# Performance work log

Hardware: AMD Instinct MI355X
Metric: run time of the kernel (lower is better)

The kernel has to match this reference:

```python
import jax, jax.numpy as jnp
import numpy as np

N_NODES = 100000
N_EDGES = 1600000
D_IN = 64
H = 64


def setup_inputs() -> dict:
    key = jax.random.key(0)
    ks = jax.random.split(key, 8)
    inp = {
        "x": jax.random.normal(ks[0], (N_NODES, D_IN), dtype=jnp.float32),
        "edge_index": jax.random.randint(ks[1], (2, N_EDGES), 0, N_NODES, dtype=jnp.int64),
        # layer 1 (SAGEConv): lin_l (aggregated neighbors, with bias), lin_r (root, no bias)
        "Wl1": jax.random.normal(ks[2], (D_IN, H), dtype=jnp.float32) / np.sqrt(D_IN),
        "bl1": jnp.zeros((H,), dtype=jnp.float32),
        "Wr1": jax.random.normal(ks[3], (D_IN, H), dtype=jnp.float32) / np.sqrt(D_IN),
        # layer 2
        "Wl2": jax.random.normal(ks[4], (H, H), dtype=jnp.float32) / np.sqrt(H),
        "bl2": jnp.zeros((H,), dtype=jnp.float32),
        "Wr2": jax.random.normal(ks[5], (H, H), dtype=jnp.float32) / np.sqrt(H),
        "Wfc": jax.random.normal(ks[6], (H, 1), dtype=jnp.float32) / np.sqrt(H),
        "bfc": jnp.zeros((1,), dtype=jnp.float32),
    }
    return inp


def _sage_conv(h, src, dst, inv_deg, Wl, bl, Wr):
    # mean-aggregate neighbor features: scatter-add messages then normalize by in-degree
    agg = jax.ops.segment_sum(h[src], dst, num_segments=N_NODES)  # [N, d]
    agg = agg * inv_deg[:, None]
    return agg @ Wl + bl + h @ Wr


def reference(x, edge_index, Wl1, bl1, Wr1, Wl2, bl2, Wr2, Wfc, bfc):
    src, dst = edge_index[0], edge_index[1]
    deg = jax.ops.segment_sum(jnp.ones((src.shape[0],), dtype=x.dtype), dst,
                              num_segments=N_NODES)
    inv_deg = jnp.where(deg > 0, 1.0 / jnp.maximum(deg, 1.0), 0.0)

    h = jax.nn.relu(_sage_conv(x, src, dst, inv_deg, Wl1, bl1, Wr1))
    h = jax.nn.relu(_sage_conv(h, src, dst, inv_deg, Wl2, bl2, Wr2))
    return h @ Wfc + bfc  # [N, 1]
```

## Files before the change

kernel.cpp:

```cpp
#include <hip/hip_runtime.h>
#include <hip/hip_fp16.h>

#define NN 100000
#define NE 1600000
#define SHIFT 8
#define NBUCK 391
#define P1B   391
#define EPB   4093

typedef _Float16 f16x8 __attribute__((ext_vector_type(8)));
typedef float f32x4 __attribute__((ext_vector_type(4)));
union H8U4 { f16x8 h; uint4 u; };

__device__ __forceinline__ int scan256(int* s, int t, int v) {
    s[t] = v;
    __syncthreads();
    for (int off = 1; off < 256; off <<= 1) {
        int add = (t >= off) ? s[t - off] : 0;
        __syncthreads();
        s[t] += add;
        __syncthreads();
    }
    return s[t];
}

__global__ __launch_bounds__(256) void k_hist(
    const float4* __restrict__ x4, ushort4* __restrict__ xh4,
    const float* __restrict__ Wl1, const float* __restrict__ Wr1, unsigned short* __restrict__ wt1,
    const float* __restrict__ Wl2, const float* __restrict__ Wr2, unsigned short* __restrict__ wt2,
    const int* __restrict__ dst, int* __restrict__ hist, int* __restrict__ bin_total)
{
    __shared__ int h[NBUCK];
    int t = threadIdx.x, blk = blockIdx.x;

    const int n4 = NN * 16;
    const int per = (n4 + P1B - 1) / P1B;
    int cb = blk * per, ce = min(cb + per, n4);
    for (int i = cb + t; i < ce; i += 256) {
        float4 f = x4[i];
        _Float16 a = (_Float16)f.x, b = (_Float16)f.y, c = (_Float16)f.z, d = (_Float16)f.w;
        ushort4 u;
        u.x = *(unsigned short*)&a; u.y = *(unsigned short*)&b;
        u.z = *(unsigned short*)&c; u.w = *(unsigned short*)&d;
        xh4[i] = u;
    }
    if (blk < 64) {
        int idx = (blk & 31) * 256 + t;
        const float* Wl = (blk < 32) ? Wl1 : Wl2;
        const float* Wr = (blk < 32) ? Wr1 : Wr2;
        unsigned short* wt = (blk < 32) ? wt1 : wt2;
        int n = idx >> 7, k = idx & 127;
        float v = (k < 64) ? Wl[k * 64 + n] : Wr[(k - 64) * 64 + n];
        _Float16 hv = (_Float16)v;
        wt[idx] = *(unsigned short*)&hv;
    }

    for (int i = t; i < NBUCK; i += 256) h[i] = 0;
    __syncthreads();
    int eb = blk * EPB, ee = min(eb + EPB, NE);
    for (int e = eb + t; e < ee; e += 256) atomicAdd(&h[dst[e] >> SHIFT], 1);
    __syncthreads();
    for (int i = t; i < NBUCK; i += 256) {
        int v = h[i];
        hist[(size_t)i * P1B + blk] = v;
        if (v) atomicAdd(&bin_total[i], v);
    }
}

__global__ __launch_bounds__(256) void k_cursor(int* __restrict__ hist, const int* __restrict__ bin_total,
                                                int* __restrict__ bucket_start, int* __restrict__ offsets) {
    __shared__ int sS[256];
    int b = blockIdx.x, t = threadIdx.x;

    int v = 0;
    for (int i = t; i < b; i += 256) v += bin_total[i];
    sS[t] = v;
    __syncthreads();
    for (int s = 128; s > 0; s >>= 1) {
        if (t < s) sS[t] += sS[t + s];
        __syncthreads();
    }
    int base = sS[0];
    __syncthreads();
    if (t == 0) bucket_start[b] = base;
    if (b == 0 && t == 0) { bucket_start[NBUCK] = NE; offsets[NN] = NE; }

    int carry = 0;
#pragma unroll
    for (int c = 0; c < 2; c++) {
        int idx = c * 256 + t;
        int hv = (idx < P1B) ? hist[(size_t)b * P1B + idx] : 0;
        int incl = scan256(sS, t, hv);
        if (idx < P1B) hist[(size_t)b * P1B + idx] = base + carry + incl - hv;
        __syncthreads();
        carry += sS[255];
        __syncthreads();
    }
}

__global__ __launch_bounds__(256) void k_scatter(const int* __restrict__ src, const int* __restrict__ dst,
                                                 const int* __restrict__ hist, unsigned int* __restrict__ pairs) {
    __shared__ int cur[NBUCK];
    int t = threadIdx.x, blk = blockIdx.x;
    for (int i = t; i < NBUCK; i += 256) cur[i] = hist[(size_t)i * P1B + blk];
    __syncthreads();
    int eb = blk * EPB, ee = min(eb + EPB, NE);
    for (int e = eb + t; e < ee; e += 256) {
        int d = dst[e];
        int pos = atomicAdd(&cur[d >> SHIFT], 1);
        pairs[pos] = (unsigned int)src[e] | ((unsigned int)(d & 255) << 17);
    }
}

__global__ __launch_bounds__(256) void k_bucket_csr(const unsigned int* __restrict__ pairs,
                                                    const int* __restrict__ bucket_start,
                                                    int* __restrict__ ssrc, int* __restrict__ offsets,
                                                    float* __restrict__ inv_deg) {
    __shared__ int cnt[256];
    __shared__ int sS[256];
    int b = blockIdx.x, t = threadIdx.x;
    cnt[t] = 0;
    __syncthreads();
    int beg = bucket_start[b], end = bucket_start[b + 1];
    for (int e = beg + t; e < end; e += 256) atomicAdd(&cnt[pairs[e] >> 17], 1);
    __syncthreads();
    int deg = cnt[t];
    int incl = scan256(sS, t, deg);
    int ex = incl - deg;
    int node = (b << SHIFT) + t;
    if (node < NN) {
        offsets[node] = beg + ex;
        inv_deg[node] = (deg > 0) ? (1.0f / (float)deg) : 0.0f;
    }
    __syncthreads();
    cnt[t] = beg + ex;
    __syncthreads();
    for (int e = beg + t; e < end; e += 256) {
        unsigned int pr = pairs[e];
        int pos = atomicAdd(&cnt[pr >> 17], 1);
        ssrc[pos] = (int)(pr & 0x1FFFFu);
    }
}

__global__ __launch_bounds__(256) void k_aggregate(const uint4* __restrict__ featq,
                                                   const int* __restrict__ ssrc,
                                                   const int* __restrict__ offsets, const float* __restrict__ inv_deg,
                                                   uint4* __restrict__ outq) {
    int pairid = blockIdx.x * 4 + (threadIdx.x >> 6);
    int node0 = pairid * 2;
    if (node0 >= NN) return;
    int node1 = node0 + 1;
    bool has1 = node1 < NN;
    int lane = threadIdx.x & 63;
    int c = lane & 7, g = lane >> 3;

    int beg0 = offsets[node0], end0 = offsets[node0 + 1];
    int beg1 = has1 ? offsets[node1] : 0, end1 = has1 ? offsets[node1 + 1] : 0;
    H8U4 acc0, acc1;
    acc0.h = (f16x8)(_Float16)0;
    acc1.h = (f16x8)(_Float16)0;
    int e0 = beg0, e1 = beg1;

    while (e0 + 16 <= end0 && e1 + 16 <= end1) {
        int i00 = ssrc[e0 + g], i01 = ssrc[e0 + 8 + g];
        int i10 = ssrc[e1 + g], i11 = ssrc[e1 + 8 + g];
        H8U4 q00, q01, q10, q11;
        q00.u = featq[(size_t)i00 * 8 + c];
        q01.u = featq[(size_t)i01 * 8 + c];
        q10.u = featq[(size_t)i10 * 8 + c];
        q11.u = featq[(size_t)i11 * 8 + c];
        acc0.h += q00.h; acc0.h += q01.h;
        acc1.h += q10.h; acc1.h += q11.h;
        e0 += 16; e1 += 16;
    }
    for (; e0 + 16 <= end0; e0 += 16) {
        int i0 = ssrc[e0 + g], i1 = ssrc[e0 + 8 + g];
        H8U4 q0, q1;
        q0.u = featq[(size_t)i0 * 8 + c];
        q1.u = featq[(size_t)i1 * 8 + c];
        acc0.h += q0.h; acc0.h += q1.h;
    }
    for (; e0 < end0; e0 += 8) {
        int m = end0 - e0;
        int idx = ssrc[e0 + (g < m ? g : m - 1)];
        H8U4 q;
        q.u = featq[(size_t)idx * 8 + c];
        if (g < m) acc0.h += q.h;
    }
    for (; e1 + 16 <= end1; e1 += 16) {
        int i0 = ssrc[e1 + g], i1 = ssrc[e1 + 8 + g];
        H8U4 q0, q1;
        q0.u = featq[(size_t)i0 * 8 + c];
        q1.u = featq[(size_t)i1 * 8 + c];
        acc1.h += q0.h; acc1.h += q1.h;
    }
    for (; e1 < end1; e1 += 8) {
        int m = end1 - e1;
        int idx = ssrc[e1 + (g < m ? g : m - 1)];
        H8U4 q;
        q.u = featq[(size_t)idx * 8 + c];
        if (g < m) acc1.h += q.h;
    }

#pragma unroll
    for (int mask = 8; mask <= 32; mask <<= 1) {
        H8U4 o0, o1;
        o0.u.x = __shfl_xor(acc0.u.x, mask); o0.u.y = __shfl_xor(acc0.u.y, mask);
        o0.u.z = __shfl_xor(acc0.u.z, mask); o0.u.w = __shfl_xor(acc0.u.w, mask);
        o1.u.x = __shfl_xor(acc1.u.x, mask); o1.u.y = __shfl_xor(acc1.u.y, mask);
        o1.u.z = __shfl_xor(acc1.u.z, mask); o1.u.w = __shfl_xor(acc1.u.w, mask);
        acc0.h += o0.h;
        acc1.h += o1.h;
    }

    if (g == 0) {
        float s0 = inv_deg[node0];
        H8U4 r;
#pragma unroll
        for (int j = 0; j < 8; j++) r.h[j] = (_Float16)((float)acc0.h[j] * s0);
        outq[(size_t)node0 * 8 + c] = r.u;
        if (has1) {
            float s1 = inv_deg[node1];
#pragma unroll
            for (int j = 0; j < 8; j++) r.h[j] = (_Float16)((float)acc1.h[j] * s1);
            outq[(size_t)node1 * 8 + c] = r.u;
        }
    }
}

template <bool FUSE_HEAD>
__global__ __launch_bounds__(256) void k_linear(const uint4* __restrict__ aggq, const uint4* __restrict__ rootq,
                                                const uint4* __restrict__ wtq,
                                                const float* __restrict__ bias,
                                                const float* __restrict__ Wfc, const float* __restrict__ bfc,
                                                float* __restrict__ out_f32, unsigned short* __restrict__ out_f16) {
    int tid = threadIdx.x;
    int wave = tid >> 6, lane = tid & 63;
    int nb = blockIdx.x * 64 + wave * 16;
    int m = lane & 15, quad = lane >> 4;

    int an = nb + m;
    if (an > NN - 1) an = NN - 1;
    H8U4 a[4];
    a[0].u = aggq[(size_t)an * 8 + quad];
    a[1].u = aggq[(size_t)an * 8 + 4 + quad];
    a[2].u = rootq[(size_t)an * 8 + quad];
    a[3].u = rootq[(size_t)an * 8 + 4 + quad];

    f32x4 acc[4];
#pragma unroll
    for (int n = 0; n < 4; n++) acc[n] = (f32x4){0.f, 0.f, 0.f, 0.f};

#pragma unroll
    for (int ncol = 0; ncol < 4; ncol++) {
        int col = ncol * 16 + m;
#pragma unroll
        for (int ki = 0; ki < 4; ki++) {
            H8U4 b;
            b.u = wtq[col * 16 + ki * 4 + quad];
            acc[ncol] = __builtin_amdgcn_mfma_f32_16x16x32_f16(a[ki].h, b.h, acc[ncol], 0, 0, 0);
        }
    }

    float bs[4];
#pragma unroll
    for (int ncol = 0; ncol < 4; ncol++) bs[ncol] = bias[ncol * 16 + m];

    if (!FUSE_HEAD) {
#pragma unroll
        for (int r = 0; r < 4; r++) {
            int node = nb + quad * 4 + r;
            if (node < NN) {
#pragma unroll
                for (int ncol = 0; ncol < 4; ncol++) {
                    float v = fmaxf(acc[ncol][r] + bs[ncol], 0.f);
                    _Float16 hv = (_Float16)v;
                    out_f16[(size_t)node * 64 + ncol * 16 + m] = *(unsigned short*)&hv;
                }
            }
        }
    } else {
        float wf[4];
#pragma unroll
        for (int ncol = 0; ncol < 4; ncol++) wf[ncol] = Wfc[ncol * 16 + m];
#pragma unroll
        for (int r = 0; r < 4; r++) {
            int node = nb + quad * 4 + r;
            float partial = 0.f;
#pragma unroll
            for (int ncol = 0; ncol < 4; ncol++)
                partial += fmaxf(acc[ncol][r] + bs[ncol], 0.f) * wf[ncol];
            partial += __shfl_xor(partial, 1);
            partial += __shfl_xor(partial, 2);
            partial += __shfl_xor(partial, 4);
            partial += __shfl_xor(partial, 8);
            if (m == 0 && node < NN) out_f32[node] = partial + bfc[0];
        }
    }
}

extern "C" void kernel_launch(void* const* d_in, const int* in_sizes, int n_in,
                              void* d_out, int out_size, void* d_ws, size_t ws_size,
                              hipStream_t stream) {
    const float* x   = (const float*)d_in[0];
    const int*   ei  = (const int*)d_in[1];
    const float* Wl1 = (const float*)d_in[2];
    const float* bl1 = (const float*)d_in[3];
    const float* Wr1 = (const float*)d_in[4];
    const float* Wl2 = (const float*)d_in[5];
    const float* bl2 = (const float*)d_in[6];
    const float* Wr2 = (const float*)d_in[7];
    const float* Wfc = (const float*)d_in[8];
    const float* bfc = (const float*)d_in[9];
    float* out = (float*)d_out;

    const int* srcp = ei;
    const int* dstp = ei + NE;

    char* p = (char*)d_ws;
    auto carve = [&](size_t bytes) {
        char* q = p;
        p += (bytes + 255) & ~size_t(255);
        return q;
    };
    int*            offsets = (int*)carve((size_t)(NN + 1) * 4);
    float*          inv_deg = (float*)carve((size_t)NN * 4);
    int*            ssrc    = (int*)carve((size_t)NE * 4);
    unsigned short* xh      = (unsigned short*)carve((size_t)NN * 64 * 2);
    unsigned short* h1h     = (unsigned short*)carve((size_t)NN * 64 * 2);
    unsigned short* aggh    = (unsigned short*)carve((size_t)NN * 64 * 2);
    unsigned short* wt1     = (unsigned short*)carve(64 * 128 * 2);
    unsigned short* wt2     = (unsigned short*)carve(64 * 128 * 2);
    unsigned int* pairs        = (unsigned int*)aggh;
    int*          hist         = (int*)(pairs + NE);
    int*          bin_total    = hist + (size_t)NBUCK * P1B;
    int*          bucket_start = bin_total + NBUCK;

    const int tile = (NN + 63) / 64;

    hipMemsetAsync(bin_total, 0, NBUCK * 4, stream);
    k_hist<<<P1B, 256, 0, stream>>>((const float4*)x, (ushort4*)xh,
                                    Wl1, Wr1, wt1, Wl2, Wr2, wt2, dstp, hist, bin_total);
    k_cursor<<<NBUCK, 256, 0, stream>>>(hist, bin_total, bucket_start, offsets);
    k_scatter<<<P1B, 256, 0, stream>>>(srcp, dstp, hist, pairs);
    k_bucket_csr<<<NBUCK, 256, 0, stream>>>(pairs, bucket_start, ssrc, offsets, inv_deg);

    const int aggblocks = ((NN + 1) / 2 + 3) / 4;
    k_aggregate<<<aggblocks, 256, 0, stream>>>((const uint4*)xh, ssrc, offsets, inv_deg, (uint4*)aggh);
    k_linear<false><<<tile, 256, 0, stream>>>((const uint4*)aggh, (const uint4*)xh, (const uint4*)wt1,
                                              bl1, Wfc, bfc, nullptr, h1h);
    k_aggregate<<<aggblocks, 256, 0, stream>>>((const uint4*)h1h, ssrc, offsets, inv_deg, (uint4*)aggh);
    k_linear<true><<<tile, 256, 0, stream>>>((const uint4*)aggh, (const uint4*)h1h, (const uint4*)wt2,
                                             bl2, Wfc, bfc, out, nullptr);
}
```

Before: 255.3 us.

## Fuse neighbor aggregation into linear layer kernel via shared memory

Each block now aggregates neighbor features for its 64 nodes into shared memory, then runs the MFMA linear transform directly, eliminating the intermediate aggregated-feature buffer and two kernel launches. Workspace buffers previously aliased onto that buffer get their own allocations. The trade-off is much less parallelism for the gather phase: each wave now processes 8 node pairs sequentially and there are far fewer blocks, reducing memory latency hiding.

```diff
diff --git a/kernel.cpp b/kernel.cpp
--- a/kernel.cpp
+++ b/kernel.cpp
@@ -142,23 +142,9 @@
     }
 }
 
-__global__ __launch_bounds__(256) void k_aggregate(const uint4* __restrict__ featq,
-                                                   const int* __restrict__ ssrc,
-                                                   const int* __restrict__ offsets, const float* __restrict__ inv_deg,
-                                                   uint4* __restrict__ outq) {
-    int pairid = blockIdx.x * 4 + (threadIdx.x >> 6);
-    int node0 = pairid * 2;
-    if (node0 >= NN) return;
-    int node1 = node0 + 1;
-    bool has1 = node1 < NN;
-    int lane = threadIdx.x & 63;
-    int c = lane & 7, g = lane >> 3;
-
-    int beg0 = offsets[node0], end0 = offsets[node0 + 1];
-    int beg1 = has1 ? offsets[node1] : 0, end1 = has1 ? offsets[node1 + 1] : 0;
-    H8U4 acc0, acc1;
-    acc0.h = (f16x8)(_Float16)0;
-    acc1.h = (f16x8)(_Float16)0;
+__device__ __forceinline__ void agg_pair(const uint4* __restrict__ featq, const int* __restrict__ ssrc,
+                                         int beg0, int end0, int beg1, int end1,
+                                         int c, int g, H8U4& acc0, H8U4& acc1) {
     int e0 = beg0, e1 = beg1;
 
     while (e0 + 16 <= end0 && e1 + 16 <= end1) {
@@ -201,51 +187,87 @@
         q.u = featq[(size_t)idx * 8 + c];
         if (g < m) acc1.h += q.h;
     }
-
-#pragma unroll
-    for (int mask = 8; mask <= 32; mask <<= 1) {
-        H8U4 o0, o1;
-        o0.u.x = __shfl_xor(acc0.u.x, mask); o0.u.y = __shfl_xor(acc0.u.y, mask);
-        o0.u.z = __shfl_xor(acc0.u.z, mask); o0.u.w = __shfl_xor(acc0.u.w, mask);
-        o1.u.x = __shfl_xor(acc1.u.x, mask); o1.u.y = __shfl_xor(acc1.u.y, mask);
-        o1.u.z = __shfl_xor(acc1.u.z, mask); o1.u.w = __shfl_xor(acc1.u.w, mask);
-        acc0.h += o0.h;
-        acc1.h += o1.h;
-    }
-
-    if (g == 0) {
-        float s0 = inv_deg[node0];
-        H8U4 r;
-#pragma unroll
-        for (int j = 0; j < 8; j++) r.h[j] = (_Float16)((float)acc0.h[j] * s0);
-        outq[(size_t)node0 * 8 + c] = r.u;
-        if (has1) {
-            float s1 = inv_deg[node1];
-#pragma unroll
-            for (int j = 0; j < 8; j++) r.h[j] = (_Float16)((float)acc1.h[j] * s1);
-            outq[(size_t)node1 * 8 + c] = r.u;
-        }
-    }
 }
 
 template <bool FUSE_HEAD>
-__global__ __launch_bounds__(256) void k_linear(const uint4* __restrict__ aggq, const uint4* __restrict__ rootq,
-                                                const uint4* __restrict__ wtq,
-                                                const float* __restrict__ bias,
-                                                const float* __restrict__ Wfc, const float* __restrict__ bfc,
-                                                float* __restrict__ out_f32, unsigned short* __restrict__ out_f16) {
+__global__ __launch_bounds__(256) void k_fused(const uint4* __restrict__ featq,
+                                               const int* __restrict__ ssrc,
+                                               const int* __restrict__ offsets, const float* __restrict__ inv_deg,
+                                               const uint4* __restrict__ wtq,
+                                               const float* __restrict__ bias,
+                                               const float* __restrict__ Wfc, const float* __restrict__ bfc,
+                                               float* __restrict__ out_f32, unsigned short* __restrict__ out_f16) {
+    __shared__ uint4 sAgg[64][9];
+
     int tid = threadIdx.x;
     int wave = tid >> 6, lane = tid & 63;
-    int nb = blockIdx.x * 64 + wave * 16;
+    int base = blockIdx.x * 64;
+
+    {
+        int c = lane & 7, g = lane >> 3;
+#pragma unroll 1
+        for (int p = 0; p < 8; ++p) {
+            int l0 = wave * 16 + p * 2;
+            int node0 = base + l0;
+            int node1 = node0 + 1;
+            if (node0 >= NN) {
+                if (g == 0) {
+                    uint4 z = {0u, 0u, 0u, 0u};
+                    sAgg[l0][c] = z;
+                    sAgg[l0 + 1][c] = z;
+                }
+                continue;
+            }
+            bool has1 = node1 < NN;
+            int beg0 = offsets[node0], end0 = offsets[node0 + 1];
+            int beg1 = has1 ? offsets[node1] : 0, end1 = has1 ? offsets[node1 + 1] : 0;
+            H8U4 acc0, acc1;
+            acc0.h = (f16x8)(_Float16)0;
+            acc1.h = (f16x8)(_Float16)0;
+            agg_pair(featq, ssrc, beg0, end0, beg1, end1, c, g, acc0, acc1);
+
+#pragma unroll
+            for (int mask = 8; mask <= 32; mask <<= 1) {
+                H8U4 o0, o1;
+                o0.u.x = __shfl_xor(acc0.u.x, mask); o0.u.y = __shfl_xor(acc0.u.y, mask);
+                o0.u.z = __shfl_xor(acc0.u.z, mask); o0.u.w = __shfl_xor(acc0.u.w, mask);
+                o1.u.x = __shfl_xor(acc1.u.x, mask); o1.u.y = __shfl_xor(acc1.u.y, mask);
+                o1.u.z = __shfl_xor(acc1.u.z, mask); o1.u.w = __shfl_xor(acc1.u.w, mask);
+                acc0.h += o0.h;
+                acc1.h += o1.h;
+            }
+
+            if (g == 0) {
+                float s0 = inv_deg[node0];
+                H8U4 r;
+#pragma unroll
+                for (int j = 0; j < 8; j++) r.h[j] = (_Float16)((float)acc0.h[j] * s0);
+                sAgg[l0][c] = r.u;
+                H8U4 r1;
+                if (has1) {
+                    float s1 = inv_deg[node1];
+#pragma unroll
+                    for (int j = 0; j < 8; j++) r1.h[j] = (_Float16)((float)acc1.h[j] * s1);
+                } else {
+                    r1.u = (uint4){0u, 0u, 0u, 0u};
+                }
+                sAgg[l0 + 1][c] = r1.u;
+            }
+        }
+    }
+    __syncthreads();
+
+    int nb = base + wave * 16;
     int m = lane & 15, quad = lane >> 4;
+    int l = wave * 16 + m;
 
     int an = nb + m;
     if (an > NN - 1) an = NN - 1;
     H8U4 a[4];
-    a[0].u = aggq[(size_t)an * 8 + quad];
-    a[1].u = aggq[(size_t)an * 8 + 4 + quad];
-    a[2].u = rootq[(size_t)an * 8 + quad];
-    a[3].u = rootq[(size_t)an * 8 + 4 + quad];
+    a[0].u = sAgg[l][quad];
+    a[1].u = sAgg[l][4 + quad];
+    a[2].u = featq[(size_t)an * 8 + quad];
+    a[3].u = featq[(size_t)an * 8 + 4 + quad];
 
     f32x4 acc[4];
 #pragma unroll
@@ -328,13 +350,12 @@
     int*            ssrc    = (int*)carve((size_t)NE * 4);
     unsigned short* xh      = (unsigned short*)carve((size_t)NN * 64 * 2);
     unsigned short* h1h     = (unsigned short*)carve((size_t)NN * 64 * 2);
-    unsigned short* aggh    = (unsigned short*)carve((size_t)NN * 64 * 2);
     unsigned short* wt1     = (unsigned short*)carve(64 * 128 * 2);
     unsigned short* wt2     = (unsigned short*)carve(64 * 128 * 2);
-    unsigned int* pairs        = (unsigned int*)aggh;
-    int*          hist         = (int*)(pairs + NE);
-    int*          bin_total    = hist + (size_t)NBUCK * P1B;
-    int*          bucket_start = bin_total + NBUCK;
+    unsigned int*   pairs   = (unsigned int*)carve((size_t)NE * 4);
+    int*            hist    = (int*)carve((size_t)NBUCK * P1B * 4);
+    int*            bin_total    = (int*)carve((size_t)NBUCK * 4);
+    int*            bucket_start = (int*)carve((size_t)(NBUCK + 1) * 4);
 
     const int tile = (NN + 63) / 64;
 
@@ -345,11 +366,8 @@
     k_scatter<<<P1B, 256, 0, stream>>>(srcp, dstp, hist, pairs);
     k_bucket_csr<<<NBUCK, 256, 0, stream>>>(pairs, bucket_start, ssrc, offsets, inv_deg);
 
-    const int aggblocks = ((NN + 1) / 2 + 3) / 4;
-    k_aggregate<<<aggblocks, 256, 0, stream>>>((const uint4*)xh, ssrc, offsets, inv_deg, (uint4*)aggh);
-    k_linear<false><<<tile, 256, 0, stream>>>((const uint4*)aggh, (const uint4*)xh, (const uint4*)wt1,
-                                              bl1, Wfc, bfc, nullptr, h1h);
-    k_aggregate<<<aggblocks, 256, 0, stream>>>((const uint4*)h1h, ssrc, offsets, inv_deg, (uint4*)aggh);
-    k_linear<true><<<tile, 256, 0, stream>>>((const uint4*)aggh, (const uint4*)h1h, (const uint4*)wt2,
-                                             bl2, Wfc, bfc, out, nullptr);
-}
+    k_fused<false><<<tile, 256, 0, stream>>>((const uint4*)xh, ssrc, offsets, inv_deg,
+                                             (const uint4*)wt1, bl1, Wfc, bfc, nullptr, h1h);
+    k_fused<true><<<tile, 256, 0, stream>>>((const uint4*)h1h, ssrc, offsets, inv_deg,
+                                            (const uint4*)wt2, bl2, Wfc, bfc, out, nullptr);
+}
```

Result: faster. 246.2 us (-3.6%).
